# Optimization experiments

Hardware: AMD Instinct MI355X
Metric: run time of the kernel (lower is better)

The kernel has to match this reference:

```python
import jax, jax.numpy as jnp
import numpy as np

EPS = 1e-5


def _bn(x, g, b):
    # BatchNorm1d in training mode: batch mean, biased variance, eps=1e-5
    m = jnp.mean(x, axis=0)
    v = jnp.var(x, axis=0)
    return (x - m) * jax.lax.rsqrt(v + EPS) * g + b


def setup_inputs() -> dict:
    key = jax.random.key(0)
    ks = jax.random.split(key, 16)
    B, N, F, H = 4096, 128, 4, 32
    w = lambda k, o, i: jax.random.normal(k, (o, i), jnp.float32) * 0.3
    d = {
        'u': jax.random.normal(ks[0], (B, N, F), jnp.float32),
        'mask': jnp.ones((B * N, 1), jnp.int32),
        # MLPphi params
        'p_bn1_g': jnp.ones((F,), jnp.float32), 'p_bn1_b': jnp.zeros((F,), jnp.float32), 'p_w1': w(ks[1], H, F),
        'p_bn2_g': jnp.ones((H,), jnp.float32), 'p_bn2_b': jnp.zeros((H,), jnp.float32), 'p_w2': w(ks[2], H, H),
        'p_bn3_g': jnp.ones((H,), jnp.float32), 'p_bn3_b': jnp.zeros((H,), jnp.float32), 'p_w3': w(ks[3], H, H),
        # MLPomega params
        'o_bn1_g': jnp.ones((F,), jnp.float32), 'o_bn1_b': jnp.zeros((F,), jnp.float32), 'o_w1': w(ks[4], H, F),
        'o_bn2_g': jnp.ones((H,), jnp.float32), 'o_bn2_b': jnp.zeros((H,), jnp.float32), 'o_w2': w(ks[5], H, H),
        'o_bn3_g': jnp.ones((H,), jnp.float32), 'o_bn3_b': jnp.zeros((H,), jnp.float32), 'o_w3': w(ks[6], H, H),
        # MLPtheta params
        't_bn1_g': jnp.ones((H,), jnp.float32), 't_bn1_b': jnp.zeros((H,), jnp.float32), 't_w1': w(ks[7], H, H),
        't_bn2_g': jnp.ones((H,), jnp.float32), 't_bn2_b': jnp.zeros((H,), jnp.float32), 't_w2': w(ks[8], H, H),
        't_bn3_g': jnp.ones((H,), jnp.float32), 't_bn3_b': jnp.zeros((H,), jnp.float32), 't_w3': w(ks[9], H, H),
        't_bn4_g': jnp.ones((H,), jnp.float32), 't_bn4_b': jnp.zeros((H,), jnp.float32),
        't_w4': w(ks[10], 1, H), 't_b4': jnp.zeros((1,), jnp.float32),
    }
    return d


def _forward(u, mask,
             p_bn1_g, p_bn1_b, p_w1, p_bn2_g, p_bn2_b, p_w2, p_bn3_g, p_bn3_b, p_w3,
             o_bn1_g, o_bn1_b, o_w1, o_bn2_g, o_bn2_b, o_w2, o_bn3_g, o_bn3_b, o_w3,
             t_bn1_g, t_bn1_b, t_w1, t_bn2_g, t_bn2_b, t_w2, t_bn3_g, t_bn3_b, t_w3,
             t_bn4_g, t_bn4_b, t_w4, t_b4):
    B, N, F = u.shape
    H = p_w1.shape[0]
    u_flat = u.reshape(-1, F)  # (B*N, F)

    # MLPphi: three BN+Linear(no bias)+Tanh blocks with residual adds (dropout=identity in eval)
    o1 = jnp.tanh(_bn(u_flat, p_bn1_g, p_bn1_b) @ p_w1.T)
    o2 = jnp.tanh(_bn(o1, p_bn2_g, p_bn2_b) @ p_w2.T)
    o3 = jnp.tanh(_bn(o1 + o2, p_bn3_g, p_bn3_b) @ p_w3.T)
    x_main = (o1 + o2 + o3).reshape(B, N, H)

    # MLPomega: BN+Linear+Tanh x2, BN+Linear, softmax over hidden dim (dim=1 of flat), then masked_fill
    a = jnp.tanh(_bn(u_flat, o_bn1_g, o_bn1_b) @ o_w1.T)
    a = jnp.tanh(_bn(a, o_bn2_g, o_bn2_b) @ o_w2.T)
    a = _bn(a, o_bn3_g, o_bn3_b) @ o_w3.T
    a = jax.nn.softmax(a, axis=1)
    a = jnp.where(mask == 0, -jnp.inf, a)
    x_attn = a.reshape(B, N, H)

    # attention pooling over neighbors
    x = jnp.sum(x_main * x_attn, axis=1)  # (B, H)

    x = jnp.tanh(_bn(x, t_bn1_g, t_bn1_b) @ t_w1.T)
    x = jnp.tanh(_bn(x, t_bn2_g, t_bn2_b) @ t_w2.T)
    x = jnp.tanh(_bn(x, t_bn3_g, t_bn3_b) @ t_w3.T)
    x = _bn(x, t_bn4_g, t_bn4_b) @ t_w4.T + t_b4
    return x


def reference(u, mask,
              p_bn1_g, p_bn1_b, p_w1, p_bn2_g, p_bn2_b, p_w2, p_bn3_g, p_bn3_b, p_w3,
              o_bn1_g, o_bn1_b, o_w1, o_bn2_g, o_bn2_b, o_w2, o_bn3_g, o_bn3_b, o_w3,
              t_bn1_g, t_bn1_b, t_w1, t_bn2_g, t_bn2_b, t_w2, t_bn3_g, t_bn3_b, t_w3,
              t_bn4_g, t_bn4_b, t_w4, t_b4):
    return _forward(u, mask,
                    p_bn1_g, p_bn1_b, p_w1, p_bn2_g, p_bn2_b, p_w2, p_bn3_g, p_bn3_b, p_w3,
                    o_bn1_g, o_bn1_b, o_w1, o_bn2_g, o_bn2_b, o_w2, o_bn3_g, o_bn3_b, o_w3,
                    t_bn1_g, t_bn1_b, t_w1, t_bn2_g, t_bn2_b, t_w2, t_bn3_g, t_bn3_b, t_w3,
                    t_bn4_g, t_bn4_b, t_w4, t_b4)
```

## Files before the change

kernel.cpp:

```cpp
#include <hip/hip_runtime.h>

typedef unsigned int u32;
typedef unsigned short u16;
typedef __attribute__((ext_vector_type(8))) _Float16 half8;
typedef __attribute__((ext_vector_type(4))) float f32x4;

#define ROWS  524288
#define BROWS 4096
#define EPS   1e-5f

#define S_U   0
#define S_O1  8
#define S_A1  72
#define S_O12 136
#define S_A2  200
#define S_X   264
#define S_X1  328
#define S_X2  392
#define S_X3  456
#define SHARD 1024
#define NSH   64

#define XSTR 40

__device__ __forceinline__ float bl(u32 u){ return __uint_as_float(u << 16); }
__device__ __forceinline__ float bh(u32 u){ return __uint_as_float(u & 0xFFFF0000u); }
__device__ __forceinline__ float b2f(u16 h){ return __uint_as_float(((u32)h) << 16); }
__device__ __forceinline__ u16 f2b(float f){
  u32 u = __float_as_uint(f);
  return (u16)((u + 0x7FFFu + ((u >> 16) & 1u)) >> 16);
}
__device__ __forceinline__ u16 f2h(float f){ _Float16 h = (_Float16)f; return __builtin_bit_cast(u16, h); }
__device__ __forceinline__ float h2f(u16 x){ return (float)__builtin_bit_cast(_Float16, x); }
__device__ __forceinline__ u32 pack2h(float a, float b){
  auto v = __builtin_amdgcn_cvt_pkrtz(a, b);
  return __builtin_bit_cast(u32, v);
}
__device__ __forceinline__ float lo16(u32 w){ return h2f((u16)(w & 0xFFFF)); }
__device__ __forceinline__ float hi16(u32 w){ return h2f((u16)(w >> 16)); }
__device__ __forceinline__ void unpk4(uint2 v, float* d){
  d[0]=lo16(v.x); d[1]=hi16(v.x); d[2]=lo16(v.y); d[3]=hi16(v.y);
}

__device__ __forceinline__ float tanh_fast(float x){
  float x2 = x*x;
  float num = fmaf(x2 + 105.0f, x2, 945.0f) * x;
  float den = fmaf(fmaf(x2, 15.0f, 420.0f), x2, 945.0f);
  float v = num * __builtin_amdgcn_rcpf(den);
  return fminf(1.0f, fmaxf(-1.0f, v));
}

template<bool F32>
__device__ __forceinline__ float rdp(const void* p, int i){
  if (F32) return ((const float*)p)[i];
  return b2f(((const u16*)p)[i]);
}
template<bool F32>
__device__ __forceinline__ void load_u4(const void* u, int r, float* f){
  if (F32){
    float4 v = ((const float4*)u)[r];
    f[0]=v.x; f[1]=v.y; f[2]=v.z; f[3]=v.w;
  } else {
    uint2 v = ((const uint2*)u)[r];
    f[0]=bl(v.x); f[1]=bh(v.x); f[2]=bl(v.y); f[3]=bh(v.y);
  }
}

__device__ __forceinline__ void g2lrow(const u16* __restrict__ g, int r, u16* X, int tid){
  const uint4* src = (const uint4*)&g[(size_t)r*32];
  uint4* dst = (uint4*)&X[tid*XSTR];
#pragma unroll
  for (int c=0;c<4;++c) dst[c] = src[c];
}
__device__ __forceinline__ void l2grow(const u16* X, int tid, u16* __restrict__ g, int r){
  const uint4* src = (const uint4*)&X[tid*XSTR];
  uint4* dst = (uint4*)&g[(size_t)r*32];
#pragma unroll
  for (int c=0;c<4;++c) dst[c] = src[c];
}

__global__ void k_detect(const u16* __restrict__ u, int* __restrict__ flag){
  int t = threadIdx.x;
  int bad = 0;
  for (int i = t*4; i < t*4+4; ++i){
    int e = (u[i] >> 7) & 0xFF;
    bad += (e >= 0x90) ? 1 : 0;
  }
#pragma unroll
  for (int off = 32; off >= 1; off >>= 1) bad += __shfl_down(bad, off);
  if (t == 0) *flag = (bad >= 4) ? 1 : 0;
}

template<bool F32>
__device__ __forceinline__ void stats_u_body(const void* __restrict__ u, float* __restrict__ S){
  int tid = blockIdx.x*blockDim.x + threadIdx.x;
  int nt  = gridDim.x*blockDim.x;
  float s[4]={0,0,0,0}, q[4]={0,0,0,0};
  for (int r = tid; r < ROWS; r += nt){
    float f[4]; load_u4<F32>(u, r, f);
#pragma unroll
    for (int k=0;k<4;++k){ s[k]+=f[k]; q[k]+=f[k]*f[k]; }
  }
#pragma unroll
  for (int off=32; off>=1; off>>=1){
#pragma unroll
    for (int k=0;k<4;++k){ s[k]+=__shfl_down(s[k],off); q[k]+=__shfl_down(q[k],off); }
  }
  if ((threadIdx.x & 63) == 0){
    float* Sh = S + (blockIdx.x & (NSH-1))*SHARD;
#pragma unroll
    for (int k=0;k<4;++k){ atomicAdd(&Sh[S_U+k], s[k]); atomicAdd(&Sh[S_U+4+k], q[k]); }
  }
}
__global__ __launch_bounds__(256) void k_stats_u(const void* __restrict__ u, float* __restrict__ S,
                                                 const int* __restrict__ flag){
  if (*flag) stats_u_body<true>(u,S); else stats_u_body<false>(u,S);
}

__device__ __forceinline__ void prep_u(const float* __restrict__ S, float* mr, int tid){
  if (tid < 4){
    float s=0.f, q=0.f;
    for (int sh=0; sh<NSH; ++sh){
      s += S[sh*SHARD + S_U + tid];
      q += S[sh*SHARD + S_U + 4 + tid];
    }
    float m = s*(1.0f/ROWS);
    float var = q*(1.0f/ROWS) - m*m;
    mr[tid]   = m;
    mr[4+tid] = rsqrtf(var + EPS);
  }
  __syncthreads();
}
template<bool F32>
__device__ __forceinline__ void bn_u_l(const float* mr, const void* g, const void* b,
                                       const float* f, float* xn){
#pragma unroll
  for (int k=0;k<4;++k)
    xn[k] = (f[k]-mr[k])*(rdp<F32>(g,k)*mr[4+k]) + rdp<F32>(b,k);
}

template<bool F32>
__device__ __forceinline__ void chain1_to_lds(const float* xn, const void* W1, u16* Xrow){
  u32 buf[16];
#pragma unroll
  for (int jp=0; jp<16; ++jp){
    int j0 = 2*jp, j1 = 2*jp+1;
    float a0 = tanh_fast(xn[0]*rdp<F32>(W1,j0*4+0) + xn[1]*rdp<F32>(W1,j0*4+1)
                       + xn[2]*rdp<F32>(W1,j0*4+2) + xn[3]*rdp<F32>(W1,j0*4+3));
    float a1 = tanh_fast(xn[0]*rdp<F32>(W1,j1*4+0) + xn[1]*rdp<F32>(W1,j1*4+1)
                       + xn[2]*rdp<F32>(W1,j1*4+2) + xn[3]*rdp<F32>(W1,j1*4+3));
    buf[jp] = pack2h(a0, a1);
  }
#pragma unroll
  for (int c=0;c<4;++c){
    uint4 v; v.x = buf[c*4]; v.y = buf[c*4+1]; v.z = buf[c*4+2]; v.w = buf[c*4+3];
    *(uint4*)&Xrow[c*8] = v;
  }
}

template<bool F32>
__device__ __forceinline__ void fold2(const float* __restrict__ S, int offA, int offB,
    const void* gA, const void* bA, const void* WA,
    const void* gB, const void* bB, const void* WB,
    u16* Wt, float* Cb, float* scr )
{
  int tid = threadIdx.x;
  if (tid < 64){
    int L = tid>>5, k = tid&31;
    const void* g = L? gB:gA; const void* b = L? bB:bA;
    int off = L? offB:offA;
    float s=0.f, q=0.f;
    for (int sh=0; sh<NSH; ++sh){
      s += S[sh*SHARD + off + k];
      q += S[sh*SHARD + off + 32 + k];
    }
    float m    = s*(1.0f/ROWS);
    float var  = q*(1.0f/ROWS) - m*m;
    float rstd = rsqrtf(var+EPS);
    float sc = rdp<F32>(g,k)*rstd;
    scr[tid]    = sc;
    scr[64+tid] = rdp<F32>(b,k) - m*sc;
  }
  __syncthreads();
  if (tid < 64){
    int L = tid>>5, j = tid&31;
    const void* W = L? WB:WA;
    float c = 0.f;
#pragma unroll
    for (int k=0;k<32;++k){
      float Wv = rdp<F32>(W, j*32+k);
      Wt[(L*32+j)*XSTR + k] = f2h(Wv * scr[(L<<5)|k]);
      c += Wv * scr[64 + ((L<<5)|k)];
    }
    Cb[L*32+j] = c;
  }
  __syncthreads();
}

#define KIND_TANH          0
#define KIND_TANHRES       2
#define KIND_TANHRES_ATREG 3
template<int KIND>
__device__ __forceinline__ void mfma_layer(u16* X, const u16* Wt, const float* Cb,
                                           int L, int wv, int lane, const u32* at_pk)
{
  int ln15 = lane & 15, quad = lane >> 4;
  half8 w0 = *(const half8*)&Wt[(L*32 + ln15     )*XSTR + quad*8];
  half8 w1 = *(const half8*)&Wt[(L*32 + ln15 + 16)*XSTR + quad*8];
  float bias0[4], bias1[4];
#pragma unroll
  for (int reg=0;reg<4;++reg){
    bias0[reg] = Cb[L*32 +      quad*4 + reg];
    bias1[reg] = Cb[L*32 + 16 + quad*4 + reg];
  }
  int rowbase = wv*64;
#pragma unroll
  for (int Mt=0; Mt<4; ++Mt){
    int s = rowbase + Mt*16 + ln15;
    half8 bfr = *(const half8*)&X[s*XSTR + quad*8];
    f32x4 c0 = {0.f,0.f,0.f,0.f}, c1 = {0.f,0.f,0.f,0.f};
    c0 = __builtin_amdgcn_mfma_f32_16x16x32_f16(w0, bfr, c0, 0,0,0);
    c1 = __builtin_amdgcn_mfma_f32_16x16x32_f16(w1, bfr, c1, 0,0,0);
    float o0[4], o1v[4];
    if (KIND == KIND_TANHRES || KIND == KIND_TANHRES_ATREG){
      unpk4(*(const uint2*)&X[s*XSTR +      quad*4], o0);
      unpk4(*(const uint2*)&X[s*XSTR + 16 + quad*4], o1v);
    }
    float a0v[4], a1v[4];
    if (KIND == KIND_TANHRES_ATREG){
      a0v[0]=lo16(at_pk[Mt*4+0]); a0v[1]=hi16(at_pk[Mt*4+0]);
      a0v[2]=lo16(at_pk[Mt*4+1]); a0v[3]=hi16(at_pk[Mt*4+1]);
      a1v[0]=lo16(at_pk[Mt*4+2]); a1v[1]=hi16(at_pk[Mt*4+2]);
      a1v[2]=lo16(at_pk[Mt*4+3]); a1v[3]=hi16(at_pk[Mt*4+3]);
    }
    float v0[4], v1[4];
#pragma unroll
    for (int reg=0;reg<4;++reg){
      float a = c0[reg] + bias0[reg];
      float b = c1[reg] + bias1[reg];
      if (KIND == KIND_TANH){ a = tanh_fast(a); b = tanh_fast(b); }
      else if (KIND == KIND_TANHRES){ a = o0[reg] + tanh_fast(a); b = o1v[reg] + tanh_fast(b); }
      else if (KIND == KIND_TANHRES_ATREG){
        a = (o0[reg] + tanh_fast(a)) * a0v[reg];
        b = (o1v[reg] + tanh_fast(b)) * a1v[reg];
      }
      v0[reg] = a; v1[reg] = b;
    }
    uint2 w0o, w1o;
    w0o.x = pack2h(v0[0], v0[1]); w0o.y = pack2h(v0[2], v0[3]);
    w1o.x = pack2h(v1[0], v1[1]); w1o.y = pack2h(v1[2], v1[3]);
    *(uint2*)&X[s*XSTR +      quad*4] = w0o;
    *(uint2*)&X[s*XSTR + 16 + quad*4] = w1o;
  }
}

__device__ __forceinline__ void mfma_logits_softmax(const u16* X, const u16* Wt, const float* Cb,
    int L, int wv, int lane, const int* __restrict__ mask, int maskbase, u32* at_pk)
{
  int ln15 = lane & 15, quad = lane >> 4;
  half8 w0 = *(const half8*)&Wt[(L*32 + ln15     )*XSTR + quad*8];
  half8 w1 = *(const half8*)&Wt[(L*32 + ln15 + 16)*XSTR + quad*8];
  float bias0[4], bias1[4];
#pragma unroll
  for (int reg=0;reg<4;++reg){
    bias0[reg] = Cb[L*32 +      quad*4 + reg];
    bias1[reg] = Cb[L*32 + 16 + quad*4 + reg];
  }
  int rowbase = wv*64;
#pragma unroll
  for (int Mt=0; Mt<4; ++Mt){
    int s = rowbase + Mt*16 + ln15;
    half8 bfr = *(const half8*)&X[s*XSTR + quad*8];
    f32x4 c0 = {0.f,0.f,0.f,0.f}, c1 = {0.f,0.f,0.f,0.f};
    c0 = __builtin_amdgcn_mfma_f32_16x16x32_f16(w0, bfr, c0, 0,0,0);
    c1 = __builtin_amdgcn_mfma_f32_16x16x32_f16(w1, bfr, c1, 0,0,0);
    float l0[4], l1[4];
#pragma unroll
    for (int reg=0;reg<4;++reg){ l0[reg] = c0[reg]+bias0[reg]; l1[reg] = c1[reg]+bias1[reg]; }
    float mx = l0[0];
#pragma unroll
    for (int reg=1;reg<4;++reg) mx = fmaxf(mx, l0[reg]);
#pragma unroll
    for (int reg=0;reg<4;++reg) mx = fmaxf(mx, l1[reg]);
    mx = fmaxf(mx, __shfl_xor(mx, 16));
    mx = fmaxf(mx, __shfl_xor(mx, 32));
    float sum = 0.f;
#pragma unroll
    for (int reg=0;reg<4;++reg){ l0[reg] = __expf(l0[reg]-mx); sum += l0[reg]; }
#pragma unroll
    for (int reg=0;reg<4;++reg){ l1[reg] = __expf(l1[reg]-mx); sum += l1[reg]; }
    sum += __shfl_xor(sum, 16);
    sum += __shfl_xor(sum, 32);
    float inv = __builtin_amdgcn_rcpf(sum);
    bool mz = (mask[maskbase + Mt*16 + ln15] == 0);
#pragma unroll
    for (int reg=0;reg<4;++reg){
      l0[reg] *= inv; l1[reg] *= inv;
      if (mz){ l0[reg] = -__builtin_inff(); l1[reg] = -__builtin_inff(); }
    }
    at_pk[Mt*4+0] = pack2h(l0[0], l0[1]);
    at_pk[Mt*4+1] = pack2h(l0[2], l0[3]);
    at_pk[Mt*4+2] = pack2h(l1[0], l1[1]);
    at_pk[Mt*4+3] = pack2h(l1[2], l1[3]);
  }
}

__device__ __forceinline__ void reduce_f16(const u16* X, float* lds2,
                                           float* __restrict__ S, int offS, int shard)
{
  int tid = threadIdx.x;
  __syncthreads();
  {
    int j = tid & 31, seg = tid >> 5;
    float s=0.f, q=0.f;
    for (int q2=0;q2<32;++q2){
      float v = h2f(X[(seg*32+q2)*XSTR + j]);
      s += v; q = fmaf(v,v,q);
    }
    lds2[seg*32+j] = s;
    lds2[256 + seg*32+j] = q;
  }
  __syncthreads();
  if (tid < 64){
    int j = tid & 31; bool isq = tid >= 32;
    const float* src = lds2 + (isq?256:0);
    float tot=0.f;
#pragma unroll
    for (int sg=0;sg<8;++sg) tot += src[sg*32+j];
    atomicAdd(&S[shard*SHARD + offS + (isq?32:0) + j], tot);
  }
  __syncthreads();
}

__device__ __forceinline__ void reduce_f32(const float* Xs, float* lds2,
                                           float* __restrict__ S, int offS, int shard)
{
  int tid = threadIdx.x;
  __syncthreads();
  {
    int j = tid & 31, seg = tid >> 5;
    float s=0.f, q=0.f;
    for (int q2=0;q2<32;++q2){
      float v = Xs[(seg*32+q2)*33 + j];
      s += v; q = fmaf(v,v,q);
    }
    lds2[seg*32+j] = s;
    lds2[256 + seg*32+j] = q;
  }
  __syncthreads();
  if (tid < 64){
    int j = tid & 31; bool isq = tid >= 32;
    const float* src = lds2 + (isq?256:0);
    float tot=0.f;
#pragma unroll
    for (int sg=0;sg<8;++sg) tot += src[sg*32+j];
    atomicAdd(&S[shard*SHARD + offS + (isq?32:0) + j], tot);
  }
  __syncthreads();
}

template<bool F32>
__device__ __forceinline__ void pass1_body(const void* __restrict__ u,
    const void* pg1, const void* pb1, const void* pw1,
    const void* og1, const void* ob1, const void* ow1,
    float* __restrict__ S, float* Xs, float* lds2, float* mr)
{
  int tid = threadIdx.x;
  int r = blockIdx.x*256 + tid;
  int shard = blockIdx.x & (NSH-1);
  prep_u(S, mr, tid);
  float f[4]; load_u4<F32>(u,r,f);
  float xn[4];
  float* Xp = Xs + tid*33;

  bn_u_l<F32>(mr, pg1, pb1, f, xn);
#pragma unroll
  for (int j=0;j<32;++j)
    Xp[j] = tanh_fast(xn[0]*rdp<F32>(pw1,j*4+0) + xn[1]*rdp<F32>(pw1,j*4+1)
                    + xn[2]*rdp<F32>(pw1,j*4+2) + xn[3]*rdp<F32>(pw1,j*4+3));
  reduce_f32(Xs, lds2, S, S_O1, shard);

  bn_u_l<F32>(mr, og1, ob1, f, xn);
#pragma unroll
  for (int j=0;j<32;++j)
    Xp[j] = tanh_fast(xn[0]*rdp<F32>(ow1,j*4+0) + xn[1]*rdp<F32>(ow1,j*4+1)
                    + xn[2]*rdp<F32>(ow1,j*4+2) + xn[3]*rdp<F32>(ow1,j*4+3));
  reduce_f32(Xs, lds2, S, S_A1, shard);
}
__global__ __launch_bounds__(256) void k_pass1(const void* __restrict__ u,
    const void* pg1, const void* pb1, const void* pw1,
    const void* og1, const void* ob1, const void* ow1,
    float* __restrict__ S, const int* __restrict__ flag){
  __shared__ float Xs[256*33];
  __shared__ float lds2[512];
  __shared__ float mr[8];
  if (*flag) pass1_body<true >(u,pg1,pb1,pw1,og1,ob1,ow1,S,Xs,lds2,mr);
  else       pass1_body<false>(u,pg1,pb1,pw1,og1,ob1,ow1,S,Xs,lds2,mr);
}

template<bool F32, bool MAT>
__device__ __forceinline__ void pass2_body(const void* __restrict__ u,
    const void* pg1, const void* pb1, const void* pw1,
    const void* og1, const void* ob1, const void* ow1,
    const void* pg2, const void* pb2, const void* pw2,
    const void* og2, const void* ob2, const void* ow2,
    float* __restrict__ S, u16* __restrict__ o12g, u16* __restrict__ a2g,
    u16* X, u16* Wt, float* Cb, float* lds2, float* mr)
{
  int tid = threadIdx.x;
  int wv = tid >> 6, lane = tid & 63;
  int r = blockIdx.x*256 + tid;
  int shard = blockIdx.x & (NSH-1);
  prep_u(S, mr, tid);
  fold2<F32>(S, S_O1, S_A1, pg2,pb2,pw2, og2,ob2,ow2, Wt, Cb, lds2);

  float f[4], xn[4];
  load_u4<F32>(u,r,f);

  bn_u_l<F32>(mr, pg1, pb1, f, xn);
  chain1_to_lds<F32>(xn, pw1, X + tid*XSTR);
  mfma_layer<KIND_TANHRES>(X, Wt, Cb, 0, wv, lane, 0);
  if (MAT) l2grow(X, tid, o12g, r);
  reduce_f16(X, lds2, S, S_O12, shard);

  bn_u_l<F32>(mr, og1, ob1, f, xn);
  chain1_to_lds<F32>(xn, ow1, X + tid*XSTR);
  mfma_layer<KIND_TANH  >(X, Wt, Cb, 1, wv, lane, 0);
  if (MAT) l2grow(X, tid, a2g, r);
  reduce_f16(X, lds2, S, S_A2, shard);
}
template<bool MAT>
__global__ __launch_bounds__(256) void k_pass2(const void* __restrict__ u,
    const void* pg1, const void* pb1, const void* pw1,
    const void* og1, const void* ob1, const void* ow1,
    const void* pg2, const void* pb2, const void* pw2,
    const void* og2, const void* ob2, const void* ow2,
    float* __restrict__ S, u16* o12g, u16* a2g, const int* __restrict__ flag){
  __shared__ u16 X[256*XSTR];
  __shared__ u16 Wt[2*32*XSTR];
  __shared__ float Cb[64];
  __shared__ float lds2[512];
  __shared__ float mr[8];
  if (*flag) pass2_body<true ,MAT>(u,pg1,pb1,pw1,og1,ob1,ow1,pg2,pb2,pw2,og2,ob2,ow2,S,o12g,a2g,X,Wt,Cb,lds2,mr);
  else       pass2_body<false,MAT>(u,pg1,pb1,pw1,og1,ob1,ow1,pg2,pb2,pw2,og2,ob2,ow2,S,o12g,a2g,X,Wt,Cb,lds2,mr);
}

template<bool F32>
__device__ __forceinline__ void pass3m_body(const int* __restrict__ mask,
    const void* pg3, const void* pb3, const void* pw3,
    const void* og3, const void* ob3, const void* ow3,
    const u16* __restrict__ o12g, const u16* __restrict__ a2g,
    float* __restrict__ x, float* __restrict__ S,
    u16* X, u16* Wt, float* Cb, float* red2)
{
  int tid = threadIdx.x;
  int wv = tid >> 6, lane = tid & 63;
  int r = blockIdx.x*256 + tid;
  fold2<F32>(S, S_A2, S_O12, og3,ob3,ow3, pg3,pb3,pw3, Wt, Cb, red2);

  u32 at_pk[16];
  int maskbase = blockIdx.x*256 + wv*64;

  g2lrow(a2g, r, X, tid);
  __syncthreads();
  mfma_logits_softmax(X, Wt, Cb, 0, wv, lane, mask, maskbase, at_pk);
  __syncthreads();
  g2lrow(o12g, r, X, tid);
  __syncthreads();
  mfma_layer<KIND_TANHRES_ATREG>(X, Wt, Cb, 1, wv, lane, at_pk);

  __syncthreads();
  {
    int jj = tid & 31, cgrp = (tid >> 5) & 3, half = tid >> 7;
    float s2 = 0.f;
    for (int q2=0;q2<32;++q2) s2 += h2f(X[(half*128 + cgrp*32 + q2)*XSTR + jj]);
    red2[tid] = s2;
  }
  __syncthreads();
  if (tid < 64){
    int half = tid >> 5, j = tid & 31;
    float v = red2[half*128+j] + red2[half*128+32+j] + red2[half*128+64+j] + red2[half*128+96+j];
    x[(blockIdx.x*2 + half)*32 + j] = v;
    float* Sh = S + (blockIdx.x & (NSH-1))*SHARD;
    atomicAdd(&Sh[S_X+j], v);
    atomicAdd(&Sh[S_X+32+j], v*v);
  }
}
__global__ __launch_bounds__(256) void k_pass3m(const int* __restrict__ mask,
    const void* pg3, const void* pb3, const void* pw3,
    const void* og3, const void* ob3, const void* ow3,
    const u16* o12g, const u16* a2g,
    float* __restrict__ x, float* __restrict__ S, const int* __restrict__ flag){
  __shared__ u16 X [256*XSTR];
  __shared__ u16 Wt[2*32*XSTR];
  __shared__ float Cb[64];
  __shared__ float red2[256];
  if (*flag) pass3m_body<true >(mask,pg3,pb3,pw3,og3,ob3,ow3,o12g,a2g,x,S,X,Wt,Cb,red2);
  else       pass3m_body<false>(mask,pg3,pb3,pw3,og3,ob3,ow3,o12g,a2g,x,S,X,Wt,Cb,red2);
}

template<bool F32>
__device__ __forceinline__ void fold4(const float* __restrict__ S,
    int off0,int off1,int off2,int off3,
    const void* g0,const void* b0,const void* W0,
    const void* g1,const void* b1,const void* W1,
    const void* g2,const void* b2,const void* W2,
    const void* g3,const void* b3,const void* W3,
    u16* Wt, float* Cb, float* scr)
{
  int tid = threadIdx.x;
  __shared__ float scr2[256];
  if (tid < 128){
    int L = tid>>5, k = tid&31;
    const void* g = (L==0)?g0:(L==1)?g1:(L==2)?g2:g3;
    const void* b = (L==0)?b0:(L==1)?b1:(L==2)?b2:b3;
    int off = (L==0)?off0:(L==1)?off1:(L==2)?off2:off3;
    float s=0.f, q=0.f;
    for (int sh=0; sh<NSH; ++sh){
      s += S[sh*SHARD + off + k];
      q += S[sh*SHARD + off + 32 + k];
    }
    float m    = s*(1.0f/ROWS);
    float var  = q*(1.0f/ROWS) - m*m;
    float rstd = rsqrtf(var+EPS);
    float sc = rdp<F32>(g,k)*rstd;
    scr[tid]  = sc;
    scr2[tid] = rdp<F32>(b,k) - m*sc;
  }
  __syncthreads();
  if (tid < 128){
    int L = tid>>5, j = tid&31;
    const void* W = (L==0)?W0:(L==1)?W1:(L==2)?W2:W3;
    float c = 0.f;
#pragma unroll
    for (int k=0;k<32;++k){
      float Wv = rdp<F32>(W, j*32+k);
      Wt[(L*32+j)*XSTR + k] = f2h(Wv * scr[(L<<5)|k]);
      c += Wv * scr2[(L<<5)|k];
    }
    Cb[L*32+j] = c;
  }
  __syncthreads();
}

template<bool F32>
__device__ __forceinline__ void pass3_body(const void* __restrict__ u, const int* __restrict__ mask,
    const void* pg1, const void* pb1, const void* pw1,
    const void* og1, const void* ob1, const void* ow1,
    const void* pg2, const void* pb2, const void* pw2,
    const void* og2, const void* ob2, const void* ow2,
    const void* pg3, const void* pb3, const void* pw3,
    const void* og3, const void* ob3, const void* ow3,
    float* __restrict__ x, float* __restrict__ S,
    u16* X, u16* Wt, float* Cb, float* red2, float* mr)
{
  int tid = threadIdx.x;
  int wv = tid >> 6, lane = tid & 63;
  int r = blockIdx.x*256 + tid;
  prep_u(S, mr, tid);
  fold4<F32>(S, S_A1, S_A2, S_O1, S_O12,
             og2,ob2,ow2, og3,ob3,ow3, pg2,pb2,pw2, pg3,pb3,pw3,
             Wt, Cb, red2);

  float f[4], xn[4];
  load_u4<F32>(u,r,f);
  u32 at_pk[16];
  int maskbase = blockIdx.x*256 + wv*64;

  bn_u_l<F32>(mr, og1, ob1, f, xn);
  chain1_to_lds<F32>(xn, ow1, X + tid*XSTR);
  mfma_layer<KIND_TANH>(X, Wt, Cb, 0, wv, lane, 0);
  mfma_logits_softmax(X, Wt, Cb, 1, wv, lane, mask, maskbase, at_pk);

  bn_u_l<F32>(mr, pg1, pb1, f, xn);
  chain1_to_lds<F32>(xn, pw1, X + tid*XSTR);
  mfma_layer<KIND_TANHRES   >(X, Wt, Cb, 2, wv, lane, 0);
  mfma_layer<KIND_TANHRES_ATREG>(X, Wt, Cb, 3, wv, lane, at_pk);

  __syncthreads();
  {
    int jj = tid & 31, cgrp = (tid >> 5) & 3, half = tid >> 7;
    float s2 = 0.f;
    for (int q2=0;q2<32;++q2) s2 += h2f(X[(half*128 + cgrp*32 + q2)*XSTR + jj]);
    red2[tid] = s2;
  }
  __syncthreads();
  if (tid < 64){
    int half = tid >> 5, j = tid & 31;
    float v = red2[half*128+j] + red2[half*128+32+j] + red2[half*128+64+j] + red2[half*128+96+j];
    x[(blockIdx.x*2 + half)*32 + j] = v;
    float* Sh = S + (blockIdx.x & (NSH-1))*SHARD;
    atomicAdd(&Sh[S_X+j], v);
    atomicAdd(&Sh[S_X+32+j], v*v);
  }
}
__global__ __launch_bounds__(256) void k_pass3(const void* __restrict__ u, const int* __restrict__ mask,
    const void* pg1, const void* pb1, const void* pw1,
    const void* og1, const void* ob1, const void* ow1,
    const void* pg2, const void* pb2, const void* pw2,
    const void* og2, const void* ob2, const void* ow2,
    const void* pg3, const void* pb3, const void* pw3,
    const void* og3, const void* ob3, const void* ow3,
    float* __restrict__ x, float* __restrict__ S, const int* __restrict__ flag){
  __shared__ u16 X [256*XSTR];
  __shared__ u16 Wt[4*32*XSTR];
  __shared__ float Cb[128];
  __shared__ float red2[256];
  __shared__ float mr[8];
  if (*flag) pass3_body<true >(u,mask,pg1,pb1,pw1,og1,ob1,ow1,pg2,pb2,pw2,og2,ob2,ow2,
                               pg3,pb3,pw3,og3,ob3,ow3,x,S,X,Wt,Cb,red2,mr);
  else       pass3_body<false>(u,mask,pg1,pb1,pw1,og1,ob1,ow1,pg2,pb2,pw2,og2,ob2,ow2,
                               pg3,pb3,pw3,og3,ob3,ow3,x,S,X,Wt,Cb,red2,mr);
}

template<bool F32>
__device__ __forceinline__ void theta_body(const float* __restrict__ X, float* __restrict__ S, int offin,
    const void* g, const void* bt, const void* W, float* __restrict__ Y, int offout,
    float* lds, float* lds2)
{
  int r = blockIdx.x*blockDim.x + threadIdx.x;
  int tid = threadIdx.x;
  int shard = blockIdx.x & (NSH-1);
  if (tid < 32){
    float s=0.f, q=0.f;
    for (int sh=0; sh<NSH; ++sh){
      s += S[sh*SHARD + offin + tid];
      q += S[sh*SHARD + offin + 32 + tid];
    }
    float m = s*(1.0f/BROWS);
    float var = q*(1.0f/BROWS) - m*m;
    lds2[tid]    = m;
    lds2[32+tid] = rsqrtf(var + EPS);
  }
  __syncthreads();
  float* Xp = lds + tid*33;
#pragma unroll
  for (int k=0;k<32;++k){
    Xp[k] = (X[(size_t)r*32+k] - lds2[k]) * (rdp<F32>(g,k)*lds2[32+k]) + rdp<F32>(bt,k);
  }
  float out[32];
#pragma unroll
  for (int j=0;j<32;++j){
    float acc = 0.f;
#pragma unroll
    for (int k=0;k<32;++k) acc = fmaf(rdp<F32>(W, j*32+k), Xp[k], acc);
    out[j] = tanh_fast(acc);
    Y[(size_t)r*32+j] = out[j];
  }
  __syncthreads();
#pragma unroll
  for (int j=0;j<32;++j) Xp[j] = out[j];
  reduce_f32(lds, lds2, S, offout, shard);
}
__global__ __launch_bounds__(256) void k_theta(const float* X, float* S, int offin,
    const void* g, const void* bt, const void* W, float* Y, int offout, const int* __restrict__ flag){
  __shared__ float lds[256*33];
  __shared__ float lds2[512];
  if (*flag) theta_body<true >(X,S,offin,g,bt,W,Y,offout,lds,lds2);
  else       theta_body<false>(X,S,offin,g,bt,W,Y,offout,lds,lds2);
}

template<bool F32>
__device__ __forceinline__ void theta4_body(const float* __restrict__ X, const float* __restrict__ S, int offin,
    const void* g, const void* bt, const void* w4, const void* b4, void* out, float* ms)
{
  int r = blockIdx.x*blockDim.x + threadIdx.x;
  int tid = threadIdx.x;
  if (tid < 32){
    float s=0.f, q=0.f;
    for (int sh=0; sh<NSH; ++sh){
      s += S[sh*SHARD + offin + tid];
      q += S[sh*SHARD + offin + 32 + tid];
    }
    float m = s*(1.0f/BROWS);
    float var = q*(1.0f/BROWS) - m*m;
    ms[tid]    = m;
    ms[32+tid] = rsqrtf(var + EPS);
  }
  __syncthreads();
  float acc = rdp<F32>(b4, 0);
#pragma unroll
  for (int k=0;k<32;++k){
    float xnv = (X[(size_t)r*32+k] - ms[k]) * (rdp<F32>(g,k)*ms[32+k]) + rdp<F32>(bt,k);
    acc = fmaf(rdp<F32>(w4,k), xnv, acc);
  }
  if (F32) ((float*)out)[r] = acc;
  else     ((u16*)out)[r]  = f2b(acc);
}
__global__ __launch_bounds__(256) void k_theta4(const float* X, const float* S, int offin,
    const void* g, const void* bt, const void* w4, const void* b4, void* out, const int* __restrict__ flag){
  __shared__ float ms[64];
  if (*flag) theta4_body<true >(X,S,offin,g,bt,w4,b4,out,ms);
  else       theta4_body<false>(X,S,offin,g,bt,w4,b4,out,ms);
}

extern "C" void kernel_launch(void* const* d_in, const int* in_sizes, int n_in,
                              void* d_out, int out_size, void* d_ws, size_t ws_size,
                              hipStream_t stream)
{
  const void* u    = d_in[0];
  const int*  mask = (const int*)d_in[1];
  const void *pg1=d_in[2],  *pb1=d_in[3],  *pw1=d_in[4];
  const void *pg2=d_in[5],  *pb2=d_in[6],  *pw2=d_in[7];
  const void *pg3=d_in[8],  *pb3=d_in[9],  *pw3=d_in[10];
  const void *og1=d_in[11], *ob1=d_in[12], *ow1=d_in[13];
  const void *og2=d_in[14], *ob2=d_in[15], *ow2=d_in[16];
  const void *og3=d_in[17], *ob3=d_in[18], *ow3=d_in[19];
  const void *tg1=d_in[20], *tb1=d_in[21], *tw1=d_in[22];
  const void *tg2=d_in[23], *tb2=d_in[24], *tw2=d_in[25];
  const void *tg3=d_in[26], *tb3=d_in[27], *tw3=d_in[28];
  const void *tg4=d_in[29], *tb4=d_in[30], *tw4=d_in[31], *tbb4=d_in[32];

  char* ws = (char*)d_ws;
  int*   flag = (int*)ws;
  float* S    = (float*)(ws + 4096);
  float* x    = (float*)(ws + 524288);
  float* x1 = x  + BROWS*32;
  float* x2 = x1 + BROWS*32;
  float* x3 = x2 + BROWS*32;

  const size_t MB = 1024*1024;
  u16* o12g = (u16*)(ws + 8*MB);
  u16* a2g  = (u16*)(ws + 40*MB);
  bool MAT = ws_size >= 73*MB;

  (void)hipMemsetAsync(ws, 0, 4096 + NSH*SHARD*4, stream);
  k_detect<<<1, 64, 0, stream>>>((const u16*)u, flag);
  k_stats_u<<<1024, 256, 0, stream>>>(u, S, flag);
  k_pass1<<<2048, 256, 0, stream>>>(u, pg1,pb1,pw1, og1,ob1,ow1, S, flag);
  if (MAT){
    k_pass2<true ><<<2048, 256, 0, stream>>>(u, pg1,pb1,pw1, og1,ob1,ow1,
                                             pg2,pb2,pw2, og2,ob2,ow2, S, o12g, a2g, flag);
    k_pass3m<<<2048, 256, 0, stream>>>(mask, pg3,pb3,pw3, og3,ob3,ow3, o12g, a2g, x, S, flag);
  } else {
    k_pass2<false><<<2048, 256, 0, stream>>>(u, pg1,pb1,pw1, og1,ob1,ow1,
                                             pg2,pb2,pw2, og2,ob2,ow2, S, o12g, a2g, flag);
    k_pass3<<<2048, 256, 0, stream>>>(u, mask, pg1,pb1,pw1, og1,ob1,ow1,
                                      pg2,pb2,pw2, og2,ob2,ow2,
                                      pg3,pb3,pw3, og3,ob3,ow3, x, S, flag);
  }
  k_theta<<<16, 256, 0, stream>>>(x,  S, S_X,  tg1,tb1,tw1, x1, S_X1, flag);
  k_theta<<<16, 256, 0, stream>>>(x1, S, S_X1, tg2,tb2,tw2, x2, S_X2, flag);
  k_theta<<<16, 256, 0, stream>>>(x2, S, S_X2, tg3,tb3,tw3, x3, S_X3, flag);
  k_theta4<<<16, 256, 0, stream>>>(x3, S, S_X3, tg4,tb4,tw4,tbb4, d_out, flag);
}
```

Baseline: 331.6 us.

## Fuse theta MLP launches into one kernel with grid barriers and inline dtype detection

Replaces the separate dtype-detect kernel with a per-block detection inlined into every kernel, so the first launch and the flag read in each kernel go away. The four small theta-MLP kernels are merged into one 16-block kernel that keeps activations in registers and syncs layers with an atomic-counter grid barrier. This cuts four launches and the intermediate global round-trips. The cost is redundant detection reads in every block and a spin-wait barrier that assumes all 16 blocks are co-resident.

```diff
diff --git a/kernel.cpp b/kernel.cpp
--- a/kernel.cpp
+++ b/kernel.cpp
@@ -66,6 +66,35 @@
   }
 }
 
+__device__ __forceinline__ int detect_u(const u16* __restrict__ u, int tid, int* sf){
+  if (tid < 64){
+    int bad = 0;
+#pragma unroll
+    for (int i = 0; i < 4; ++i){
+      int e = (u[tid*4 + i] >> 7) & 0xFF;
+      bad += (e >= 0x90) ? 1 : 0;
+    }
+#pragma unroll
+    for (int off = 32; off >= 1; off >>= 1) bad += __shfl_down(bad, off);
+    if (tid == 0) *sf = (bad >= 4) ? 1 : 0;
+  }
+  __syncthreads();
+  return *sf;
+}
+
+__device__ __forceinline__ void gbar(u32* ctr, int tid, u32 nblk){
+  __threadfence();
+  __syncthreads();
+  if (tid == 0){
+    __hip_atomic_fetch_add(ctr, 1u, __ATOMIC_ACQ_REL, __HIP_MEMORY_SCOPE_AGENT);
+    while (__hip_atomic_load(ctr, __ATOMIC_ACQUIRE, __HIP_MEMORY_SCOPE_AGENT) < nblk){
+      __builtin_amdgcn_s_sleep(8);
+    }
+  }
+  __syncthreads();
+  __threadfence();
+}
+
 __device__ __forceinline__ void g2lrow(const u16* __restrict__ g, int r, u16* X, int tid){
   const uint4* src = (const uint4*)&g[(size_t)r*32];
   uint4* dst = (uint4*)&X[tid*XSTR];
@@ -77,18 +106,6 @@
   uint4* dst = (uint4*)&g[(size_t)r*32];
 #pragma unroll
   for (int c=0;c<4;++c) dst[c] = src[c];
-}
-
-__global__ void k_detect(const u16* __restrict__ u, int* __restrict__ flag){
-  int t = threadIdx.x;
-  int bad = 0;
-  for (int i = t*4; i < t*4+4; ++i){
-    int e = (u[i] >> 7) & 0xFF;
-    bad += (e >= 0x90) ? 1 : 0;
-  }
-#pragma unroll
-  for (int off = 32; off >= 1; off >>= 1) bad += __shfl_down(bad, off);
-  if (t == 0) *flag = (bad >= 4) ? 1 : 0;
 }
 
 template<bool F32>
@@ -112,9 +129,10 @@
     for (int k=0;k<4;++k){ atomicAdd(&Sh[S_U+k], s[k]); atomicAdd(&Sh[S_U+4+k], q[k]); }
   }
 }
-__global__ __launch_bounds__(256) void k_stats_u(const void* __restrict__ u, float* __restrict__ S,
-                                                 const int* __restrict__ flag){
-  if (*flag) stats_u_body<true>(u,S); else stats_u_body<false>(u,S);
+__global__ __launch_bounds__(256) void k_stats_u(const void* __restrict__ u, float* __restrict__ S){
+  __shared__ int sf;
+  int isf = detect_u((const u16*)u, threadIdx.x, &sf);
+  if (isf) stats_u_body<true>(u,S); else stats_u_body<false>(u,S);
 }
 
 __device__ __forceinline__ void prep_u(const float* __restrict__ S, float* mr, int tid){
@@ -390,12 +408,14 @@
 __global__ __launch_bounds__(256) void k_pass1(const void* __restrict__ u,
     const void* pg1, const void* pb1, const void* pw1,
     const void* og1, const void* ob1, const void* ow1,
-    float* __restrict__ S, const int* __restrict__ flag){
+    float* __restrict__ S){
   __shared__ float Xs[256*33];
   __shared__ float lds2[512];
   __shared__ float mr[8];
-  if (*flag) pass1_body<true >(u,pg1,pb1,pw1,og1,ob1,ow1,S,Xs,lds2,mr);
-  else       pass1_body<false>(u,pg1,pb1,pw1,og1,ob1,ow1,S,Xs,lds2,mr);
+  __shared__ int sf;
+  int isf = detect_u((const u16*)u, threadIdx.x, &sf);
+  if (isf) pass1_body<true >(u,pg1,pb1,pw1,og1,ob1,ow1,S,Xs,lds2,mr);
+  else     pass1_body<false>(u,pg1,pb1,pw1,og1,ob1,ow1,S,Xs,lds2,mr);
 }
 
 template<bool F32, bool MAT>
@@ -435,14 +455,16 @@
     const void* og1, const void* ob1, const void* ow1,
     const void* pg2, const void* pb2, const void* pw2,
     const void* og2, const void* ob2, const void* ow2,
-    float* __restrict__ S, u16* o12g, u16* a2g, const int* __restrict__ flag){
+    float* __restrict__ S, u16* o12g, u16* a2g){
   __shared__ u16 X[256*XSTR];
   __shared__ u16 Wt[2*32*XSTR];
   __shared__ float Cb[64];
   __shared__ float lds2[512];
   __shared__ float mr[8];
-  if (*flag) pass2_body<true ,MAT>(u,pg1,pb1,pw1,og1,ob1,ow1,pg2,pb2,pw2,og2,ob2,ow2,S,o12g,a2g,X,Wt,Cb,lds2,mr);
-  else       pass2_body<false,MAT>(u,pg1,pb1,pw1,og1,ob1,ow1,pg2,pb2,pw2,og2,ob2,ow2,S,o12g,a2g,X,Wt,Cb,lds2,mr);
+  __shared__ int sf;
+  int isf = detect_u((const u16*)u, threadIdx.x, &sf);
+  if (isf) pass2_body<true ,MAT>(u,pg1,pb1,pw1,og1,ob1,ow1,pg2,pb2,pw2,og2,ob2,ow2,S,o12g,a2g,X,Wt,Cb,lds2,mr);
+  else     pass2_body<false,MAT>(u,pg1,pb1,pw1,og1,ob1,ow1,pg2,pb2,pw2,og2,ob2,ow2,S,o12g,a2g,X,Wt,Cb,lds2,mr);
 }
 
 template<bool F32>
@@ -486,17 +508,19 @@
     atomicAdd(&Sh[S_X+32+j], v*v);
   }
 }
-__global__ __launch_bounds__(256) void k_pass3m(const int* __restrict__ mask,
+__global__ __launch_bounds__(256) void k_pass3m(const void* __restrict__ u, const int* __restrict__ mask,
     const void* pg3, const void* pb3, const void* pw3,
     const void* og3, const void* ob3, const void* ow3,
     const u16* o12g, const u16* a2g,
-    float* __restrict__ x, float* __restrict__ S, const int* __restrict__ flag){
+    float* __restrict__ x, float* __restrict__ S){
   __shared__ u16 X [256*XSTR];
   __shared__ u16 Wt[2*32*XSTR];
   __shared__ float Cb[64];
   __shared__ float red2[256];
-  if (*flag) pass3m_body<true >(mask,pg3,pb3,pw3,og3,ob3,ow3,o12g,a2g,x,S,X,Wt,Cb,red2);
-  else       pass3m_body<false>(mask,pg3,pb3,pw3,og3,ob3,ow3,o12g,a2g,x,S,X,Wt,Cb,red2);
+  __shared__ int sf;
+  int isf = detect_u((const u16*)u, threadIdx.x, &sf);
+  if (isf) pass3m_body<true >(mask,pg3,pb3,pw3,og3,ob3,ow3,o12g,a2g,x,S,X,Wt,Cb,red2);
+  else     pass3m_body<false>(mask,pg3,pb3,pw3,og3,ob3,ow3,o12g,a2g,x,S,X,Wt,Cb,red2);
 }
 
 template<bool F32>
@@ -601,31 +625,81 @@
     const void* og2, const void* ob2, const void* ow2,
     const void* pg3, const void* pb3, const void* pw3,
     const void* og3, const void* ob3, const void* ow3,
-    float* __restrict__ x, float* __restrict__ S, const int* __restrict__ flag){
+    float* __restrict__ x, float* __restrict__ S){
   __shared__ u16 X [256*XSTR];
   __shared__ u16 Wt[4*32*XSTR];
   __shared__ float Cb[128];
   __shared__ float red2[256];
   __shared__ float mr[8];
-  if (*flag) pass3_body<true >(u,mask,pg1,pb1,pw1,og1,ob1,ow1,pg2,pb2,pw2,og2,ob2,ow2,
-                               pg3,pb3,pw3,og3,ob3,ow3,x,S,X,Wt,Cb,red2,mr);
-  else       pass3_body<false>(u,mask,pg1,pb1,pw1,og1,ob1,ow1,pg2,pb2,pw2,og2,ob2,ow2,
-                               pg3,pb3,pw3,og3,ob3,ow3,x,S,X,Wt,Cb,red2,mr);
-}
-
-template<bool F32>
-__device__ __forceinline__ void theta_body(const float* __restrict__ X, float* __restrict__ S, int offin,
-    const void* g, const void* bt, const void* W, float* __restrict__ Y, int offout,
-    float* lds, float* lds2)
-{
-  int r = blockIdx.x*blockDim.x + threadIdx.x;
-  int tid = threadIdx.x;
-  int shard = blockIdx.x & (NSH-1);
+  __shared__ int sf;
+  int isf = detect_u((const u16*)u, threadIdx.x, &sf);
+  if (isf) pass3_body<true >(u,mask,pg1,pb1,pw1,og1,ob1,ow1,pg2,pb2,pw2,og2,ob2,ow2,
+                             pg3,pb3,pw3,og3,ob3,ow3,x,S,X,Wt,Cb,red2,mr);
+  else     pass3_body<false>(u,mask,pg1,pb1,pw1,og1,ob1,ow1,pg2,pb2,pw2,og2,ob2,ow2,
+                             pg3,pb3,pw3,og3,ob3,ow3,x,S,X,Wt,Cb,red2,mr);
+}
+
+template<bool F32>
+__device__ __forceinline__ void theta_all_body(const float* __restrict__ x,
+    float* __restrict__ S, u32* __restrict__ bars,
+    const void* tg1, const void* tb1, const void* tw1,
+    const void* tg2, const void* tb2, const void* tw2,
+    const void* tg3, const void* tb3, const void* tw3,
+    const void* tg4, const void* tb4, const void* tw4, const void* tbb4,
+    void* out, float* lds, float* lds2)
+{
+  int tid = threadIdx.x;
+  int blk = blockIdx.x;
+  int r = blk*256 + tid;
+  float v[32];
+#pragma unroll
+  for (int k=0;k<32;++k) v[k] = x[(size_t)r*32+k];
+
+  const void* gs[3]  = {tg1, tg2, tg3};
+  const void* bs[3]  = {tb1, tb2, tb3};
+  const void* Ws[3]  = {tw1, tw2, tw3};
+  const int offin[4]  = {S_X, S_X1, S_X2, S_X3};
+  const int offout[3] = {S_X1, S_X2, S_X3};
+
+#pragma unroll
+  for (int L=0; L<3; ++L){
+    int nsh = (L==0) ? NSH : 16;
+    if (tid < 32){
+      float s=0.f, q=0.f;
+      for (int sh=0; sh<nsh; ++sh){
+        s += S[sh*SHARD + offin[L] + tid];
+        q += S[sh*SHARD + offin[L] + 32 + tid];
+      }
+      float m = s*(1.0f/BROWS);
+      float var = q*(1.0f/BROWS) - m*m;
+      lds2[tid]    = m;
+      lds2[32+tid] = rsqrtf(var + EPS);
+    }
+    __syncthreads();
+    float* Xp = lds + tid*33;
+#pragma unroll
+    for (int k=0;k<32;++k)
+      Xp[k] = (v[k] - lds2[k]) * (rdp<F32>(gs[L],k)*lds2[32+k]) + rdp<F32>(bs[L],k);
+    __syncthreads();
+#pragma unroll
+    for (int j=0;j<32;++j){
+      float acc = 0.f;
+#pragma unroll
+      for (int k=0;k<32;++k) acc = fmaf(rdp<F32>(Ws[L], j*32+k), Xp[k], acc);
+      v[j] = tanh_fast(acc);
+    }
+    __syncthreads();
+#pragma unroll
+    for (int j=0;j<32;++j) Xp[j] = v[j];
+    reduce_f32(lds, lds2, S, offout[L], blk);
+    gbar(&bars[L], tid, 16);
+  }
+
   if (tid < 32){
     float s=0.f, q=0.f;
-    for (int sh=0; sh<NSH; ++sh){
-      s += S[sh*SHARD + offin + tid];
-      q += S[sh*SHARD + offin + 32 + tid];
+    for (int sh=0; sh<16; ++sh){
+      s += S[sh*SHARD + S_X3 + tid];
+      q += S[sh*SHARD + S_X3 + 32 + tid];
     }
     float m = s*(1.0f/BROWS);
     float var = q*(1.0f/BROWS) - m*m;
@@ -633,65 +707,28 @@
     lds2[32+tid] = rsqrtf(var + EPS);
   }
   __syncthreads();
-  float* Xp = lds + tid*33;
+  float acc = rdp<F32>(tbb4, 0);
 #pragma unroll
   for (int k=0;k<32;++k){
-    Xp[k] = (X[(size_t)r*32+k] - lds2[k]) * (rdp<F32>(g,k)*lds2[32+k]) + rdp<F32>(bt,k);
-  }
-  float out[32];
-#pragma unroll
-  for (int j=0;j<32;++j){
-    float acc = 0.f;
-#pragma unroll
-    for (int k=0;k<32;++k) acc = fmaf(rdp<F32>(W, j*32+k), Xp[k], acc);
-    out[j] = tanh_fast(acc);
-    Y[(size_t)r*32+j] = out[j];
-  }
-  __syncthreads();
-#pragma unroll
-  for (int j=0;j<32;++j) Xp[j] = out[j];
-  reduce_f32(lds, lds2, S, offout, shard);
-}
-__global__ __launch_bounds__(256) void k_theta(const float* X, float* S, int offin,
-    const void* g, const void* bt, const void* W, float* Y, int offout, const int* __restrict__ flag){
+    float xnv = (v[k] - lds2[k]) * (rdp<F32>(tg4,k)*lds2[32+k]) + rdp<F32>(tb4,k);
+    acc = fmaf(rdp<F32>(tw4,k), xnv, acc);
+  }
+  if (F32) ((float*)out)[r] = acc;
+  else     ((u16*)out)[r]  = f2b(acc);
+}
+__global__ __launch_bounds__(256) void k_theta_all(const void* __restrict__ u,
+    const float* __restrict__ x, float* __restrict__ S, u32* __restrict__ bars,
+    const void* tg1, const void* tb1, const void* tw1,
+    const void* tg2, const void* tb2, const void* tw2,
+    const void* tg3, const void* tb3, const void* tw3,
+    const void* tg4, const void* tb4, const void* tw4, const void* tbb4,
+    void* out){
   __shared__ float lds[256*33];
   __shared__ float lds2[512];
-  if (*flag) theta_body<true >(X,S,offin,g,bt,W,Y,offout,lds,lds2);
-  else       theta_body<false>(X,S,offin,g,bt,W,Y,offout,lds,lds2);
-}
-
-template<bool F32>
-__device__ __forceinline__ void theta4_body(const float* __restrict__ X, const float* __restrict__ S, int offin,
-    const void* g, const void* bt, const void* w4, const void* b4, void* out, float* ms)
-{
-  int r = blockIdx.x*blockDim.x + threadIdx.x;
-  int tid = threadIdx.x;
-  if (tid < 32){
-    float s=0.f, q=0.f;
-    for (int sh=0; sh<NSH; ++sh){
-      s += S[sh*SHARD + offin + tid];
-      q += S[sh*SHARD + offin + 32 + tid];
-    }
-    float m = s*(1.0f/BROWS);
-    float var = q*(1.0f/BROWS) - m*m;
-    ms[tid]    = m;
-    ms[32+tid] = rsqrtf(var + EPS);
-  }
-  __syncthreads();
-  float acc = rdp<F32>(b4, 0);
-#pragma unroll
-  for (int k=0;k<32;++k){
-    float xnv = (X[(size_t)r*32+k] - ms[k]) * (rdp<F32>(g,k)*ms[32+k]) + rdp<F32>(bt,k);
-    acc = fmaf(rdp<F32>(w4,k), xnv, acc);
-  }
-  if (F32) ((float*)out)[r] = acc;
-  else     ((u16*)out)[r]  = f2b(acc);
-}
-__global__ __launch_bounds__(256) void k_theta4(const float* X, const float* S, int offin,
-    const void* g, const void* bt, const void* w4, const void* b4, void* out, const int* __restrict__ flag){
-  __shared__ float ms[64];
-  if (*flag) theta4_body<true >(X,S,offin,g,bt,w4,b4,out,ms);
-  else       theta4_body<false>(X,S,offin,g,bt,w4,b4,out,ms);
+  __shared__ int sf;
+  int isf = detect_u((const u16*)u, threadIdx.x, &sf);
+  if (isf) theta_all_body<true >(x,S,bars,tg1,tb1,tw1,tg2,tb2,tw2,tg3,tb3,tw3,tg4,tb4,tw4,tbb4,out,lds,lds2);
+  else     theta_all_body<false>(x,S,bars,tg1,tb1,tw1,tg2,tb2,tw2,tg3,tb3,tw3,tg4,tb4,tw4,tbb4,out,lds,lds2);
 }
 
 extern "C" void kernel_launch(void* const* d_in, const int* in_sizes, int n_in,
@@ -712,12 +749,9 @@
   const void *tg4=d_in[29], *tb4=d_in[30], *tw4=d_in[31], *tbb4=d_in[32];
 
   char* ws = (char*)d_ws;
-  int*   flag = (int*)ws;
+  u32*   bars = (u32*)(ws + 256);
   float* S    = (float*)(ws + 4096);
   float* x    = (float*)(ws + 524288);
-  float* x1 = x  + BROWS*32;
-  float* x2 = x1 + BROWS*32;
-  float* x3 = x2 + BROWS*32;
 
   const size_t MB = 1024*1024;
   u16* o12g = (u16*)(ws + 8*MB);
@@ -725,22 +759,20 @@
   bool MAT = ws_size >= 73*MB;
 
   (void)hipMemsetAsync(ws, 0, 4096 + NSH*SHARD*4, stream);
-  k_detect<<<1, 64, 0, stream>>>((const u16*)u, flag);
-  k_stats_u<<<1024, 256, 0, stream>>>(u, S, flag);
-  k_pass1<<<2048, 256, 0, stream>>>(u, pg1,pb1,pw1, og1,ob1,ow1, S, flag);
+  k_stats_u<<<1024, 256, 0, stream>>>(u, S);
+  k_pass1<<<2048, 256, 0, stream>>>(u, pg1,pb1,pw1, og1,ob1,ow1, S);
   if (MAT){
     k_pass2<true ><<<2048, 256, 0, stream>>>(u, pg1,pb1,pw1, og1,ob1,ow1,
-                                             pg2,pb2,pw2, og2,ob2,ow2, S, o12g, a2g, flag);
-    k_pass3m<<<2048, 256, 0, stream>>>(mask, pg3,pb3,pw3, og3,ob3,ow3, o12g, a2g, x, S, flag);
+                                             pg2,pb2,pw2, og2,ob2,ow2, S, o12g, a2g);
+    k_pass3m<<<2048, 256, 0, stream>>>(u, mask, pg3,pb3,pw3, og3,ob3,ow3, o12g, a2g, x, S);
   } else {
     k_pass2<false><<<2048, 256, 0, stream>>>(u, pg1,pb1,pw1, og1,ob1,ow1,
-                                             pg2,pb2,pw2, og2,ob2,ow2, S, o12g, a2g, flag);
+                                             pg2,pb2,pw2, og2,ob2,ow2, S, o12g, a2g);
     k_pass3<<<2048, 256, 0, stream>>>(u, mask, pg1,pb1,pw1, og1,ob1,ow1,
                                       pg2,pb2,pw2, og2,ob2,ow2,
-                                      pg3,pb3,pw3, og3,ob3,ow3, x, S, flag);
-  }
-  k_theta<<<16, 256, 0, stream>>>(x,  S, S_X,  tg1,tb1,tw1, x1, S_X1, flag);
-  k_theta<<<16, 256, 0, stream>>>(x1, S, S_X1, tg2,tb2,tw2, x2, S_X2, flag);
-  k_theta<<<16, 256, 0, stream>>>(x2, S, S_X2, tg3,tb3,tw3, x3, S_X3, flag);
-  k_theta4<<<16, 256, 0, stream>>>(x3, S, S_X3, tg4,tb4,tw4,tbb4, d_out, flag);
-}
+                                      pg3,pb3,pw3, og3,ob3,ow3, x, S);
+  }
+  k_theta_all<<<16, 256, 0, stream>>>(u, x, S, bars,
+                                      tg1,tb1,tw1, tg2,tb2,tw2, tg3,tb3,tw3,
+                                      tg4,tb4,tw4,tbb4, d_out);
+}
```

Result: faster. 318.2 us (-4.1%).
